# Performance work log

Measured on AMD Instinct MI355X. Metric: run time of the kernel, lower is better.

The kernel has to match this reference:

```python
import jax, jax.numpy as jnp
import numpy as np

N_NODES = 10000
N_EDGES = 160000
DIM = 128
NLAYERS = 3
NBASIS = 16
NSPECIES = 100
CUTOFF = 5.0


def _mlp(x, W1, b1, W2, b2):
    # FullyConnectedNet([hidden, out]) with silu on hidden, linear output
    return jax.nn.silu(x @ W1 + b1) @ W2 + b2


def setup_inputs() -> dict:
    key = jax.random.key(0)
    ks = iter(jax.random.split(key, 64))
    scale = 0.08

    def w(shape):
        return jax.random.normal(next(ks), shape, dtype=jnp.float32) * scale

    inp = {
        "species": jax.random.randint(next(ks), (N_NODES,), 0, NSPECIES, dtype=jnp.int32),
        "edge_src": jnp.sort(jax.random.randint(next(ks), (N_EDGES,), 0, N_NODES, dtype=jnp.int32)),
        "edge_dst": jax.random.randint(next(ks), (N_EDGES,), 0, N_NODES, dtype=jnp.int32),
        "distances": 0.5 + 4.4 * jax.random.uniform(next(ks), (N_EDGES,), dtype=jnp.float32),
        "vec": jax.random.normal(next(ks), (N_EDGES, 3), dtype=jnp.float32),
        "switch": jax.random.uniform(next(ks), (N_EDGES,), dtype=jnp.float32),
        "species_W": w((NSPECIES, DIM)),
        "species_b": w((DIM,)),
        "radial_W": w((NLAYERS, NBASIS, DIM)),
        "radial_b": w((NLAYERS, DIM)),
    }
    for nm, out in [("a", DIM), ("F", 1), ("f", DIM), ("R", DIM), ("r", DIM), ("u", DIM)]:
        inp[nm + "_W1"] = w((NLAYERS, DIM, DIM))
        inp[nm + "_b1"] = w((NLAYERS, DIM))
        inp[nm + "_W2"] = w((NLAYERS, DIM, out))
        inp[nm + "_b2"] = w((NLAYERS, out))
    return inp


def reference(species, edge_src, edge_dst, distances, vec, switch,
              species_W, species_b, radial_W, radial_b,
              a_W1, a_b1, a_W2, a_b2,
              F_W1, F_b1, F_W2, F_b2,
              f_W1, f_b1, f_W2, f_b2,
              R_W1, R_b1, R_W2, R_b2,
              r_W1, r_b1, r_W2, r_b2,
              u_W1, u_b1, u_W2, u_b2):
    N = species.shape[0]
    # species encoding -> species_linear Dense
    xi = jax.nn.one_hot(species, NSPECIES, dtype=jnp.float32) @ species_W + species_b  # (N, dim)
    sw = switch[:, None]                                   # (E, 1)
    dirij = vec / distances[:, None] * sw                  # (E, 3)
    # gaussian radial basis on [0, cutoff]
    centers = jnp.linspace(0.0, CUTOFF, NBASIS, dtype=jnp.float32)
    eta = jnp.float32((NBASIS / CUTOFF) ** 2)
    rb = jnp.exp(-eta * (distances[:, None] - centers) ** 2)  # (E, nbasis)

    fi = None
    di = None
    for l in range(NLAYERS):
        ai = _mlp(xi, a_W1[l], a_b1[l], a_W2[l], a_b2[l])          # (N, dim)
        Dij = rb @ radial_W[l] + radial_b[l]                        # (E, dim)
        mij = ai[edge_src] * ai[edge_dst] * Dij * sw                # (E, dim)
        xi = xi + jax.ops.segment_sum(mij, edge_src, N)
        Fij = _mlp(mij, F_W1[l], F_b1[l], F_W2[l], F_b2[l]) * dirij  # (E, 3)
        fij = _mlp(mij, f_W1[l], f_b1[l], f_W2[l], f_b2[l])[:, :, None] * Fij[:, None, :]  # (E, C, 3)
        fij_sum = jax.ops.segment_sum(fij, edge_src, N)             # (N, C, 3)
        fi = fij_sum if l == 0 else fi + fij_sum
        deltai = _mlp(xi, R_W1[l], R_b1[l], R_W2[l], R_b2[l])[:, :, None] * fi  # (N, C, 3)
        if l == 0:
            di = deltai
        else:
            phi_rij = _mlp(mij, r_W1[l], r_b1[l], r_W2[l], r_b2[l])  # (E, C)
            phi_r = jax.ops.segment_sum(phi_rij * sw, edge_src, N)   # (N, C)
            di = phi_r[:, :, None] * di + deltai
        scal = jnp.sum(fi * di, axis=-1)                             # (N, C)
        dui = -_mlp(xi, u_W1[l], u_b1[l], u_W2[l], u_b2[l]) * scal   # (N, dim) since C == dim
        xi = xi + dui
    return xi
```

## Files before the change

kernel.cpp:

```cpp
#include <hip/hip_runtime.h>
#include <hip/hip_bf16.h>

#define N_NODES 10000
#define N_EDGES 160000
#define DIM     128
#define NBASIS  16
#define LDT     136
#define NFE     (N_NODES*DIM)

typedef __bf16 bf16x8 __attribute__((ext_vector_type(8)));
typedef __bf16 bf16x4 __attribute__((ext_vector_type(4)));
typedef __bf16 bf16x2 __attribute__((ext_vector_type(2)));
typedef float  f32x4  __attribute__((ext_vector_type(4)));

__device__ __forceinline__ float silu_f(float x){
  return x * (1.0f / (1.0f + __expf(-x)));
}
__device__ __forceinline__ f32x4 mfma16(bf16x8 a, bf16x8 b, f32x4 c){
  return __builtin_amdgcn_mfma_f32_16x16x32_bf16(a,b,c,0,0,0);
}


struct WPtrs { const float* p[11]; };

template<bool WITH_R>
__global__ __launch_bounds__(256,2) void mlp_layer(
    int nodeB,
    const __bf16* __restrict__ mij,
    const int*    __restrict__ esrc, const float* __restrict__ dirv,
    const __bf16* __restrict__ fW1z, const float* __restrict__ fb1,
    const __bf16* __restrict__ fW2z, const float* __restrict__ fb2,
    const __bf16* __restrict__ FW1z, const float* __restrict__ Fb1,
    const float*  __restrict__ FW2v, const float* __restrict__ Fb2,
    const __bf16* __restrict__ rW1z, const float* __restrict__ rb1,
    const __bf16* __restrict__ rW2z, const float* __restrict__ rb2,
    const float*  __restrict__ swv,
    float* __restrict__ fiG, float* __restrict__ phiG,
    const float* __restrict__ X,
    const __bf16* __restrict__ RW1z, const float* __restrict__ Rb1,
    const __bf16* __restrict__ RW2z, const float* __restrict__ Rb2,
    const __bf16* __restrict__ uW1z, const float* __restrict__ ub1,
    const __bf16* __restrict__ uW2z, const float* __restrict__ ub2,
    float* __restrict__ Rv, float* __restrict__ uv)
{
  __shared__ __bf16 sH[128*LDT];
  __shared__ __bf16 sW[2][8192];
  __shared__ int    sE[128];
  __shared__ float  sDir[128*3];
  const int tid=threadIdx.x, lane=tid&63, wv=tid>>6, l15=lane&15, quad=lane>>4;

  if ((int)blockIdx.x < nodeB){
    const long row0n = (long)blockIdx.x*64 + wv*16;
    const long rA = row0n + l15;
    const bool okA = rA < N_NODES;

    bf16x8 fa[4];
    #pragma unroll
    for (int kc=0;kc<4;kc++){
      int kb=kc*32+quad*8;
      bf16x8 a;
      #pragma unroll
      for (int i=0;i<8;i++) a[i]=(__bf16)0.f;
      if (okA){
        float4 u0 = *(const float4*)(X + rA*DIM + kb);
        float4 u1 = *(const float4*)(X + rA*DIM + kb + 4);
        a[0]=(__bf16)u0.x;a[1]=(__bf16)u0.y;a[2]=(__bf16)u0.z;a[3]=(__bf16)u0.w;
        a[4]=(__bf16)u1.x;a[5]=(__bf16)u1.y;a[6]=(__bf16)u1.z;a[7]=(__bf16)u1.w;
      }
      fa[kc]=a;
    }

    f32x4 acc[8];
    auto zacc = [&](){
      #pragma unroll
      for (int ni=0;ni<8;++ni) acc[ni]=(f32x4){0.f,0.f,0.f,0.f};
    };
    auto gemmA = [&](const __bf16* __restrict__ Wz){
      #pragma unroll
      for (int kc=0;kc<4;kc++){
        #pragma unroll
        for (int ni=0;ni<8;ni++){
          bf16x8 w = *(const bf16x8*)(Wz + (long)(kc*512 + ni*64 + lane)*8);
          acc[ni]=mfma16(w,fa[kc],acc[ni]);
        }
      }
    };
    auto gemmH = [&](const __bf16* __restrict__ Wz){
      #pragma unroll
      for (int kc=0;kc<4;kc++){
        bf16x8 h0=*(bf16x8*)&sH[(wv*16+l15)*LDT + kc*32 + quad*8];
        #pragma unroll
        for (int ni=0;ni<8;ni++){
          bf16x8 w = *(const bf16x8*)(Wz + (long)(kc*512 + ni*64 + lane)*8);
          acc[ni]=mfma16(w,h0,acc[ni]);
        }
      }
    };
    auto hEpi = [&](const float* __restrict__ b1){
      #pragma unroll
      for (int ni=0;ni<8;++ni){
        int n0 = ni*16 + quad*4;
        float4 bb = *(const float4*)(b1 + n0);
        bf16x4 h;
        h[0]=(__bf16)silu_f(acc[ni][0]+bb.x);
        h[1]=(__bf16)silu_f(acc[ni][1]+bb.y);
        h[2]=(__bf16)silu_f(acc[ni][2]+bb.z);
        h[3]=(__bf16)silu_f(acc[ni][3]+bb.w);
        *(bf16x4*)&sH[(wv*16+l15)*LDT + n0] = h;
      }
    };
    auto cStoreF = [&](const float* __restrict__ b2, float* __restrict__ Y){
      if (okA){
        #pragma unroll
        for (int ni=0;ni<8;++ni){
          int n0 = ni*16 + quad*4;
          float4 bb = *(const float4*)(b2 + n0);
          float4 o;
          o.x=acc[ni][0]+bb.x; o.y=acc[ni][1]+bb.y;
          o.z=acc[ni][2]+bb.z; o.w=acc[ni][3]+bb.w;
          *(float4*)(Y + rA*DIM + n0) = o;
        }
      }
    };

    zacc(); gemmA(RW1z); hEpi(Rb1);
    zacc(); gemmH(RW2z); cStoreF(Rb2, Rv);
    zacc(); gemmA(uW1z); hEpi(ub1);
    zacc(); gemmH(uW2z); cStoreF(ub2, uv);
    return;
  }

  const long row0 = (long)(blockIdx.x - nodeB)*128;
  const int  rloc0 = wv*32 + l15;
  const long rB0 = row0 + rloc0, rB1 = rB0+16;

  if (tid < 32)  *(int4*)&sE[tid*4]    = *(const int4*)(esrc + row0 + tid*4);
  if (tid >= 64 && tid < 160)
    *(float4*)&sDir[(tid-64)*4] = *(const float4*)(dirv + row0*3 + (tid-64)*4);

  bf16x8 fb[2][4];
  #pragma unroll
  for (int kc=0;kc<4;kc++){
    fb[0][kc] = *(const bf16x8*)(mij + rB0*DIM + kc*32 + quad*8);
    fb[1][kc] = *(const bf16x8*)(mij + rB1*DIM + kc*32 + quad*8);
  }
  float swr[2];
  if constexpr (WITH_R){ swr[0]=swv[rB0]; swr[1]=swv[rB1]; }

  f32x4 acc[2][8];
  bf16x8 pre[4];
  float eF[2];

  auto preload = [&](const __bf16* __restrict__ Wz, int half){
    #pragma unroll
    for (int it=0; it<4; ++it)
      pre[it] = *(const bf16x8*)(Wz + (long)(half*1024 + it*256 + tid)*8);
  };
  auto writePre = [&](int b){
    #pragma unroll
    for (int it=0; it<4; ++it)
      *(bf16x8*)&sW[b][(it*256+tid)*8] = pre[it];
  };
  auto zacc = [&](){
    #pragma unroll
    for (int mi=0;mi<2;++mi)
      #pragma unroll
      for (int ni=0;ni<8;++ni) acc[mi][ni]=(f32x4){0.f,0.f,0.f,0.f};
  };
  auto mfmaB = [&](int b, int half){
    #pragma unroll
    for (int k2=0;k2<2;k2++){
      int kc = half*2 + k2;
      #pragma unroll
      for (int ni=0;ni<8;ni++){
        bf16x8 w = *(bf16x8*)&sW[b][(k2*512 + ni*64 + lane)*8];
        acc[0][ni]=mfma16(w,fb[0][kc],acc[0][ni]);
        acc[1][ni]=mfma16(w,fb[1][kc],acc[1][ni]);
      }
    }
  };
  auto mfmaH = [&](int b, int half){
    #pragma unroll
    for (int k2=0;k2<2;k2++){
      int kc = half*2 + k2;
      bf16x8 h0=*(bf16x8*)&sH[(rloc0   )*LDT + kc*32 + quad*8];
      bf16x8 h1=*(bf16x8*)&sH[(rloc0+16)*LDT + kc*32 + quad*8];
      #pragma unroll
      for (int ni=0;ni<8;ni++){
        bf16x8 w = *(bf16x8*)&sW[b][(k2*512 + ni*64 + lane)*8];
        acc[0][ni]=mfma16(w,h0,acc[0][ni]);
        acc[1][ni]=mfma16(w,h1,acc[1][ni]);
      }
    }
  };
  auto fEpi = [&](){
    float fb2v = Fb2[0];
    #pragma unroll
    for (int mi=0;mi<2;++mi){
      float p = 0.f;
      #pragma unroll
      for (int ni=0;ni<8;++ni){
        int n0 = ni*16 + quad*4;
        float4 bb = *(const float4*)(Fb1 + n0);
        float4 w2 = *(const float4*)(FW2v + n0);
        p += silu_f(acc[mi][ni][0]+bb.x)*w2.x;
        p += silu_f(acc[mi][ni][1]+bb.y)*w2.y;
        p += silu_f(acc[mi][ni][2]+bb.z)*w2.z;
        p += silu_f(acc[mi][ni][3]+bb.w)*w2.w;
      }
      p += __shfl_xor(p,16);
      p += __shfl_xor(p,32);
      eF[mi] = p + fb2v;
    }
  };
  auto hEpi = [&](const float* __restrict__ b1){
    #pragma unroll
    for (int mi=0;mi<2;++mi){
      int rl = wv*32 + mi*16 + l15;
      #pragma unroll
      for (int ni=0;ni<8;++ni){
        int n0 = ni*16 + quad*4;
        float4 bb = *(const float4*)(b1 + n0);
        bf16x4 h;
        h[0]=(__bf16)silu_f(acc[mi][ni][0]+bb.x);
        h[1]=(__bf16)silu_f(acc[mi][ni][1]+bb.y);
        h[2]=(__bf16)silu_f(acc[mi][ni][2]+bb.z);
        h[3]=(__bf16)silu_f(acc[mi][ni][3]+bb.w);
        *(bf16x4*)&sH[rl*LDT + n0] = h;
      }
    }
  };
  auto outLDS = [&](const float* __restrict__ b2, const float* mul){
    #pragma unroll
    for (int mi=0;mi<2;++mi){
      int rl = wv*32 + mi*16 + l15;
      #pragma unroll
      for (int ni=0;ni<8;++ni){
        int n0 = ni*16 + quad*4;
        float4 bb = *(const float4*)(b2 + n0);
        bf16x4 o;
        o[0]=(__bf16)((acc[mi][ni][0]+bb.x)*mul[mi]);
        o[1]=(__bf16)((acc[mi][ni][1]+bb.y)*mul[mi]);
        o[2]=(__bf16)((acc[mi][ni][2]+bb.z)*mul[mi]);
        o[3]=(__bf16)((acc[mi][ni][3]+bb.w)*mul[mi]);
        *(bf16x4*)&sH[rl*LDT + n0] = o;
      }
    }
  };
  auto reduceFi = [&](){
    const int d = lane*2;
    float a0=0.f,a1=0.f,a2=0.f,a3=0.f,a4=0.f,a5=0.f;
    int cur = sE[wv*32];
    for (int i=0;i<32;i++){
      int e = wv*32+i;
      int n = sE[e];
      if (n != cur){
        long b = (long)cur*DIM + d;
        atomicAdd(&fiG[0L*NFE + b  ], a0);
        atomicAdd(&fiG[0L*NFE + b+1], a3);
        atomicAdd(&fiG[1L*NFE + b  ], a1);
        atomicAdd(&fiG[1L*NFE + b+1], a4);
        atomicAdd(&fiG[2L*NFE + b  ], a2);
        atomicAdd(&fiG[2L*NFE + b+1], a5);
        a0=a1=a2=a3=a4=a5=0.f; cur=n;
      }
      bf16x2 v = *(bf16x2*)&sH[e*LDT + d];
      float vx=(float)v[0], vy=(float)v[1];
      float d0=sDir[e*3+0], d1=sDir[e*3+1], d2=sDir[e*3+2];
      a0+=vx*d0; a1+=vx*d1; a2+=vx*d2;
      a3+=vy*d0; a4+=vy*d1; a5+=vy*d2;
    }
    long b = (long)cur*DIM + d;
    atomicAdd(&fiG[0L*NFE + b  ], a0);
    atomicAdd(&fiG[0L*NFE + b+1], a3);
    atomicAdd(&fiG[1L*NFE + b  ], a1);
    atomicAdd(&fiG[1L*NFE + b+1], a4);
    atomicAdd(&fiG[2L*NFE + b  ], a2);
    atomicAdd(&fiG[2L*NFE + b+1], a5);
  };
  auto reducePhi = [&](){
    const int d = lane*2;
    float a0=0.f,a1=0.f;
    int cur = sE[wv*32];
    for (int i=0;i<32;i++){
      int e = wv*32+i;
      int n = sE[e];
      if (n != cur){
        atomicAdd(&phiG[(long)cur*DIM + d  ], a0);
        atomicAdd(&phiG[(long)cur*DIM + d+1], a1);
        a0=a1=0.f; cur=n;
      }
      bf16x2 v = *(bf16x2*)&sH[e*LDT + d];
      a0 += (float)v[0]; a1 += (float)v[1];
    }
    atomicAdd(&phiG[(long)cur*DIM + d  ], a0);
    atomicAdd(&phiG[(long)cur*DIM + d+1], a1);
  };

  preload(FW1z,0); writePre(0);
  __syncthreads();
  preload(FW1z,1);
  zacc(); mfmaB(0,0);
  writePre(1);
  __syncthreads();
  preload(fW1z,0);
  mfmaB(1,1);
  writePre(0);
  __syncthreads();
  preload(fW1z,1);
  fEpi();
  zacc(); mfmaB(0,0);
  writePre(1);
  __syncthreads();
  preload(fW2z,0);
  mfmaB(1,1);
  writePre(0);
  __syncthreads();
  preload(fW2z,1);
  hEpi(fb1);
  zacc(); mfmaH(0,0);
  writePre(1);
  __syncthreads();
  if constexpr (WITH_R) preload(rW1z,0);
  mfmaH(1,1);
  outLDS(fb2, eF);
  reduceFi();

  if constexpr (WITH_R){
    writePre(0);
    __syncthreads();
    preload(rW1z,1);
    zacc(); mfmaB(0,0);
    writePre(1);
    __syncthreads();
    preload(rW2z,0);
    mfmaB(1,1);
    writePre(0);
    __syncthreads();
    preload(rW2z,1);
    hEpi(rb1);
    zacc(); mfmaH(0,0);
    writePre(1);
    __syncthreads();
    mfmaH(1,1);
    outLDS(rb2, swr);
    reducePhi();
  }
}

__global__ __launch_bounds__(64,4) void mlp_a(
    const float* __restrict__ X,
    const __bf16* __restrict__ W1z, const float* __restrict__ b1,
    const __bf16* __restrict__ W2z, const float* __restrict__ b2,
    __bf16* __restrict__ Y)
{
  __shared__ __bf16 sH[16*LDT];
  const int lane=threadIdx.x, l15=lane&15, quad=lane>>4;
  const long row0=(long)blockIdx.x*16;
  const long rA=row0+l15;

  bf16x8 fa[4];
  #pragma unroll
  for (int kc=0;kc<4;kc++){
    int kb=kc*32+quad*8;
    float4 u0 = *(const float4*)(X + rA*DIM + kb);
    float4 u1 = *(const float4*)(X + rA*DIM + kb + 4);
    bf16x8 a;
    a[0]=(__bf16)u0.x;a[1]=(__bf16)u0.y;a[2]=(__bf16)u0.z;a[3]=(__bf16)u0.w;
    a[4]=(__bf16)u1.x;a[5]=(__bf16)u1.y;a[6]=(__bf16)u1.z;a[7]=(__bf16)u1.w;
    fa[kc]=a;
  }

  f32x4 acc[8];
  #pragma unroll
  for (int ni=0;ni<8;++ni) acc[ni]=(f32x4){0.f,0.f,0.f,0.f};
  #pragma unroll
  for (int kc=0;kc<4;kc++){
    #pragma unroll
    for (int ni=0;ni<8;ni++){
      bf16x8 w = *(const bf16x8*)(W1z + (long)(kc*512 + ni*64 + lane)*8);
      acc[ni]=mfma16(w,fa[kc],acc[ni]);
    }
  }
  #pragma unroll
  for (int ni=0;ni<8;++ni){
    int n0 = ni*16 + quad*4;
    float4 bb = *(const float4*)(b1 + n0);
    bf16x4 h;
    h[0]=(__bf16)silu_f(acc[ni][0]+bb.x);
    h[1]=(__bf16)silu_f(acc[ni][1]+bb.y);
    h[2]=(__bf16)silu_f(acc[ni][2]+bb.z);
    h[3]=(__bf16)silu_f(acc[ni][3]+bb.w);
    *(bf16x4*)&sH[l15*LDT + n0] = h;
  }
  #pragma unroll
  for (int ni=0;ni<8;++ni) acc[ni]=(f32x4){0.f,0.f,0.f,0.f};
  #pragma unroll
  for (int kc=0;kc<4;kc++){
    bf16x8 h0=*(bf16x8*)&sH[l15*LDT + kc*32 + quad*8];
    #pragma unroll
    for (int ni=0;ni<8;ni++){
      bf16x8 w = *(const bf16x8*)(W2z + (long)(kc*512 + ni*64 + lane)*8);
      acc[ni]=mfma16(w,h0,acc[ni]);
    }
  }
  #pragma unroll
  for (int ni=0;ni<8;++ni){
    int n0 = ni*16 + quad*4;
    float4 bb = *(const float4*)(b2 + n0);
    bf16x4 o;
    o[0]=(__bf16)(acc[ni][0]+bb.x);
    o[1]=(__bf16)(acc[ni][1]+bb.y);
    o[2]=(__bf16)(acc[ni][2]+bb.z);
    o[3]=(__bf16)(acc[ni][3]+bb.w);
    *(bf16x4*)(Y + rA*DIM + n0) = o;
  }
}

__global__ __launch_bounds__(256) void setup_all(
    WPtrs wp, __bf16* __restrict__ wt,
    const int* __restrict__ species, const float* __restrict__ spW,
    const float* __restrict__ spB, float* __restrict__ xi, float* __restrict__ fi,
    float* __restrict__ phi,
    const float* __restrict__ dist, const float* __restrict__ vec,
    const float* __restrict__ swv, float* __restrict__ dir, float* __restrict__ rb)
{
  const int b = blockIdx.x, tid = threadIdx.x;
  if (b < 33){
    int t = b/3, l = b%3;
    const float* src = wp.p[t] + (size_t)l*16384;
    __bf16* out = wt + (size_t)b*16384;
    for (int it=0; it<8; ++it){
      int fi_ = it*256 + tid;
      int kc = fi_>>9, ni = (fi_>>6)&7, lane = fi_&63;
      int n  = ni*16 + (lane&15);
      int k0 = kc*32 + (lane>>4)*8;
      bf16x8 v;
      #pragma unroll
      for (int j=0;j<8;++j) v[j] = (__bf16)src[(k0+j)*DIM + n];
      *(bf16x8*)(out + (size_t)fi_*8) = v;
    }
  } else if (b < 33 + 5000){
    int idx = (b-33)*256 + tid;
    int n = idx >> 7, d = idx & 127;
    xi[idx] = spW[species[n]*DIM + d] + spB[d];
    phi[idx] = 0.f;
    fi[idx] = 0.f;
    fi[NFE + idx] = 0.f;
    fi[2L*NFE + idx] = 0.f;
  } else {
    int e = (b-5033)*256 + tid;
    if (e < N_EDGES){
      float d = dist[e];
      float s = swv[e];
      float inv = s / d;
      dir[e*3+0] = vec[e*3+0]*inv;
      dir[e*3+1] = vec[e*3+1]*inv;
      dir[e*3+2] = vec[e*3+2]*inv;
      const float eta = (16.0f/5.0f)*(16.0f/5.0f);
      #pragma unroll
      for (int j=0;j<NBASIS;j++){
        float c = (float)j * (5.0f/15.0f);
        float t2 = d - c;
        rb[e*NBASIS + j] = __expf(-eta*t2*t2);
      }
    }
  }
}

__global__ __launch_bounds__(256) void mij_segsum(
    const __bf16* __restrict__ ai, const int* __restrict__ esrc, const int* __restrict__ edst,
    const float* __restrict__ swv, const float* __restrict__ rb,
    const float* __restrict__ radW, const float* __restrict__ radB,
    __bf16* __restrict__ mij, float* __restrict__ xi)
{
  __shared__ float sRb[64*NBASIS];
  __shared__ int   sS[64], sD[64];
  __shared__ float sSw[64];
  int tid = threadIdx.x;
  int e0 = blockIdx.x * 64;
  *(float4*)(sRb + tid*4) = *(const float4*)(rb + (long)e0*NBASIS + tid*4);
  if (tid < 64){
    sS[tid]  = esrc[e0+tid];
    sD[tid]  = edst[e0+tid];
    sSw[tid] = swv[e0+tid];
  }
  const int wv = tid>>6, lane = tid&63;
  const int d = lane*2;
  float2 rw[NBASIS];
  #pragma unroll
  for (int j=0;j<NBASIS;j++)
    rw[j] = *(const float2*)(radW + j*DIM + d);
  float2 rB = *(const float2*)(radB + d);
  __syncthreads();

  float sx=0.f, sy=0.f;
  int cur = sS[wv*16];
  #pragma unroll
  for (int i=0;i<16;i++){
    int el = wv*16 + i;
    int n = sS[el];
    if (n != cur){
      atomicAdd(&xi[(long)cur*DIM+d  ], sx);
      atomicAdd(&xi[(long)cur*DIM+d+1], sy);
      sx=0.f; sy=0.f; cur=n;
    }
    bf16x2 as = *(const bf16x2*)(ai + (long)n*DIM + d);
    bf16x2 ad = *(const bf16x2*)(ai + (long)sD[el]*DIM + d);
    float acc0 = 0.f, acc1 = 0.f;
    #pragma unroll
    for (int j=0;j<NBASIS;j++){
      float rbv = sRb[el*NBASIS+j];
      acc0 += rbv*rw[j].x;
      acc1 += rbv*rw[j].y;
    }
    float sw_ = sSw[el];
    float m0 = (float)as[0]*(float)ad[0]*(acc0+rB.x)*sw_;
    float m1 = (float)as[1]*(float)ad[1]*(acc1+rB.y)*sw_;
    bf16x2 m; m[0]=(__bf16)m0; m[1]=(__bf16)m1;
    *(bf16x2*)(mij + (long)(e0+el)*DIM + d) = m;
    sx += m0; sy += m1;
  }
  atomicAdd(&xi[(long)cur*DIM+d  ], sx);
  atomicAdd(&xi[(long)cur*DIM+d+1], sy);
}

__global__ __launch_bounds__(256) void node_update(
    const float* __restrict__ Rv, const float* __restrict__ uv,
    float* __restrict__ fi, float* __restrict__ di, float* __restrict__ xi,
    float* __restrict__ phi, float* __restrict__ out, int layer)
{
  long idx = (long)blockIdx.x*256 + threadIdx.x;
  float f0 = fi[idx];
  float f1 = fi[NFE + idx];
  float f2 = fi[2L*NFE + idx];
  float phi_v = (layer > 0) ? phi[idx] : 0.f;
  float Rv_ = Rv[idx];
  float fv[3] = {f0,f1,f2};
  float sc = 0.f;
  #pragma unroll
  for (int k=0;k<3;k++){
    float delta = Rv_*fv[k];
    float dv = (layer==0) ? delta : phi_v*di[(long)k*NFE + idx] + delta;
    di[(long)k*NFE + idx] = dv;
    sc += fv[k]*dv;
  }
  float nx = xi[idx] - uv[idx]*sc;
  xi[idx] = nx;
  phi[idx] = 0.f;
  if (layer == 2) out[idx] = nx;
}

extern "C" void kernel_launch(void* const* d_in, const int* in_sizes, int n_in,
                              void* d_out, int out_size, void* d_ws, size_t ws_size,
                              hipStream_t stream) {
  const int*   species = (const int*)  d_in[0];
  const int*   esrc    = (const int*)  d_in[1];
  const int*   edst    = (const int*)  d_in[2];
  const float* dist    = (const float*)d_in[3];
  const float* vec     = (const float*)d_in[4];
  const float* swv     = (const float*)d_in[5];
  const float* spW     = (const float*)d_in[6];
  const float* spB     = (const float*)d_in[7];
  const float* radW    = (const float*)d_in[8];
  const float* radB    = (const float*)d_in[9];
  const float* aW1=(const float*)d_in[10], *aB1=(const float*)d_in[11], *aW2=(const float*)d_in[12], *aB2=(const float*)d_in[13];
  const float* FW1=(const float*)d_in[14], *FB1=(const float*)d_in[15], *FW2=(const float*)d_in[16], *FB2=(const float*)d_in[17];
  const float* fW1=(const float*)d_in[18], *fB1=(const float*)d_in[19], *fW2=(const float*)d_in[20], *fB2=(const float*)d_in[21];
  const float* RW1=(const float*)d_in[22], *RB1=(const float*)d_in[23], *RW2=(const float*)d_in[24], *RB2=(const float*)d_in[25];
  const float* rW1=(const float*)d_in[26], *rB1=(const float*)d_in[27], *rW2=(const float*)d_in[28], *rB2=(const float*)d_in[29];
  const float* uW1=(const float*)d_in[30], *uB1=(const float*)d_in[31], *uW2=(const float*)d_in[32], *uB2=(const float*)d_in[33];

  const long NF = (long)N_NODES*DIM;
  const long EF = (long)N_EDGES*DIM;
  float* ws   = (float*)d_ws;
  float* xi   = ws;
  float* Rv   = xi   + NF;
  float* uv   = Rv   + NF;
  float* phi  = uv   + NF;
  float* fi   = phi  + NF;
  float* di   = fi   + 3*NF;
  float* dir  = di   + 3*NF;
  float* rb   = dir  + 3L*N_EDGES;
  char* bp = (char*)(rb + 16L*N_EDGES);
  size_t off = ((size_t)(bp - (char*)d_ws) + 15) & ~(size_t)15;
  __bf16* ai   = (__bf16*)((char*)d_ws + off);
  __bf16* mij  = ai  + NF;
  __bf16* wt   = mij + EF;

  WPtrs wp;
  wp.p[0]=aW1; wp.p[1]=aW2; wp.p[2]=FW1; wp.p[3]=fW1; wp.p[4]=fW2;
  wp.p[5]=RW1; wp.p[6]=RW2; wp.p[7]=rW1; wp.p[8]=rW2; wp.p[9]=uW1; wp.p[10]=uW2;

  setup_all<<<5658, 256, 0, stream>>>(wp, wt,
                                      species, spW, spB, xi, fi, phi,
                                      dist, vec, swv, dir, rb);

  const int nodeB = (N_NODES + 63)/64;
  const int edgeB = N_EDGES/128;
  #define WT(t,l) (wt + (size_t)((t)*3+(l))*16384)

  for (int l=0;l<3;l++){
    const long bo = (long)l*DIM;

    mlp_a<<<N_NODES/16, 64, 0, stream>>>(xi, WT(0,l), aB1+bo, WT(1,l), aB2+bo, ai);
    mij_segsum<<<N_EDGES/64, 256, 0, stream>>>(ai, esrc, edst, swv, rb,
                                               radW + (long)l*NBASIS*DIM, radB + bo,
                                               mij, xi);
    if (l == 0)
      mlp_layer<false><<<nodeB+edgeB, 256, 0, stream>>>(
          nodeB, mij, esrc, dir,
          WT(3,l), fB1+bo, WT(4,l), fB2+bo,
          WT(2,l), FB1+bo, FW2+(long)l*DIM, FB2+l,
          nullptr, nullptr, nullptr, nullptr, nullptr,
          fi, phi,
          xi, WT(5,l), RB1+bo, WT(6,l), RB2+bo,
          WT(9,l), uB1+bo, WT(10,l), uB2+bo, Rv, uv);
    else
      mlp_layer<true><<<nodeB+edgeB, 256, 0, stream>>>(
          nodeB, mij, esrc, dir,
          WT(3,l), fB1+bo, WT(4,l), fB2+bo,
          WT(2,l), FB1+bo, FW2+(long)l*DIM, FB2+l,
          WT(7,l), rB1+bo, WT(8,l), rB2+bo, swv,
          fi, phi,
          xi, WT(5,l), RB1+bo, WT(6,l), RB2+bo,
          WT(9,l), uB1+bo, WT(10,l), uB2+bo, Rv, uv);
    node_update<<<5000, 256, 0, stream>>>(Rv, uv, fi, di, xi, phi,
                                          (float*)d_out, l);
  }
}
```

Baseline: 502.3 us.

## Read MLP weights directly from global memory and drop LDS double-buffering

The edge-MLP path no longer stages weight tiles through a double-buffered shared-memory array with per-stage barriers. Each wave now loads weight fragments straight from global memory, relying on L1/L2 caching. This cuts shared-memory use so the launch bound can rise to 4 blocks per CU and removes most barriers. The cost is that every wave fetches the full weight matrices separately, which adds cache traffic. Direction vectors are also padded to float4 in shared memory so each edge needs one vector load, and one barrier is added after the index and direction staging.

```diff
diff --git a/kernel.cpp b/kernel.cpp
--- a/kernel.cpp
+++ b/kernel.cpp
@@ -24,7 +24,7 @@
 struct WPtrs { const float* p[11]; };
 
 template<bool WITH_R>
-__global__ __launch_bounds__(256,2) void mlp_layer(
+__global__ __launch_bounds__(256,4) void mlp_layer(
     int nodeB,
     const __bf16* __restrict__ mij,
     const int*    __restrict__ esrc, const float* __restrict__ dirv,
@@ -44,9 +44,8 @@
     float* __restrict__ Rv, float* __restrict__ uv)
 {
   __shared__ __bf16 sH[128*LDT];
-  __shared__ __bf16 sW[2][8192];
   __shared__ int    sE[128];
-  __shared__ float  sDir[128*3];
+  __shared__ float  sDir[128*4];
   const int tid=threadIdx.x, lane=tid&63, wv=tid>>6, l15=lane&15, quad=lane>>4;
 
   if ((int)blockIdx.x < nodeB){
@@ -134,9 +133,13 @@
   const int  rloc0 = wv*32 + l15;
   const long rB0 = row0 + rloc0, rB1 = rB0+16;
 
-  if (tid < 32)  *(int4*)&sE[tid*4]    = *(const int4*)(esrc + row0 + tid*4);
-  if (tid >= 64 && tid < 160)
-    *(float4*)&sDir[(tid-64)*4] = *(const float4*)(dirv + row0*3 + (tid-64)*4);
+  if (tid < 32)  *(int4*)&sE[tid*4] = *(const int4*)(esrc + row0 + tid*4);
+  if (tid >= 128){
+    int t = tid - 128;
+    long e3 = (row0 + t)*3;
+    float d0 = dirv[e3+0], d1 = dirv[e3+1], d2 = dirv[e3+2];
+    *(float4*)&sDir[t*4] = (float4){d0,d1,d2,0.f};
+  }
 
   bf16x8 fb[2][4];
   #pragma unroll
@@ -147,47 +150,36 @@
   float swr[2];
   if constexpr (WITH_R){ swr[0]=swv[rB0]; swr[1]=swv[rB1]; }
 
+  __syncthreads();
+
   f32x4 acc[2][8];
-  bf16x8 pre[4];
   float eF[2];
 
-  auto preload = [&](const __bf16* __restrict__ Wz, int half){
-    #pragma unroll
-    for (int it=0; it<4; ++it)
-      pre[it] = *(const bf16x8*)(Wz + (long)(half*1024 + it*256 + tid)*8);
-  };
-  auto writePre = [&](int b){
-    #pragma unroll
-    for (int it=0; it<4; ++it)
-      *(bf16x8*)&sW[b][(it*256+tid)*8] = pre[it];
-  };
   auto zacc = [&](){
     #pragma unroll
     for (int mi=0;mi<2;++mi)
       #pragma unroll
       for (int ni=0;ni<8;++ni) acc[mi][ni]=(f32x4){0.f,0.f,0.f,0.f};
   };
-  auto mfmaB = [&](int b, int half){
-    #pragma unroll
-    for (int k2=0;k2<2;k2++){
-      int kc = half*2 + k2;
+  auto gemmG = [&](const __bf16* __restrict__ Wz){
+    #pragma unroll
+    for (int kc=0;kc<4;kc++){
       #pragma unroll
       for (int ni=0;ni<8;ni++){
-        bf16x8 w = *(bf16x8*)&sW[b][(k2*512 + ni*64 + lane)*8];
+        bf16x8 w = *(const bf16x8*)(Wz + (long)(kc*512 + ni*64 + lane)*8);
         acc[0][ni]=mfma16(w,fb[0][kc],acc[0][ni]);
         acc[1][ni]=mfma16(w,fb[1][kc],acc[1][ni]);
       }
     }
   };
-  auto mfmaH = [&](int b, int half){
-    #pragma unroll
-    for (int k2=0;k2<2;k2++){
-      int kc = half*2 + k2;
+  auto gemmHG = [&](const __bf16* __restrict__ Wz){
+    #pragma unroll
+    for (int kc=0;kc<4;kc++){
       bf16x8 h0=*(bf16x8*)&sH[(rloc0   )*LDT + kc*32 + quad*8];
       bf16x8 h1=*(bf16x8*)&sH[(rloc0+16)*LDT + kc*32 + quad*8];
       #pragma unroll
       for (int ni=0;ni<8;ni++){
-        bf16x8 w = *(bf16x8*)&sW[b][(k2*512 + ni*64 + lane)*8];
+        bf16x8 w = *(const bf16x8*)(Wz + (long)(kc*512 + ni*64 + lane)*8);
         acc[0][ni]=mfma16(w,h0,acc[0][ni]);
         acc[1][ni]=mfma16(w,h1,acc[1][ni]);
       }
@@ -266,9 +258,9 @@
       }
       bf16x2 v = *(bf16x2*)&sH[e*LDT + d];
       float vx=(float)v[0], vy=(float)v[1];
-      float d0=sDir[e*3+0], d1=sDir[e*3+1], d2=sDir[e*3+2];
-      a0+=vx*d0; a1+=vx*d1; a2+=vx*d2;
-      a3+=vy*d0; a4+=vy*d1; a5+=vy*d2;
+      float4 dv = *(float4*)&sDir[e*4];
+      a0+=vx*dv.x; a1+=vx*dv.y; a2+=vx*dv.z;
+      a3+=vy*dv.x; a4+=vy*dv.y; a5+=vy*dv.z;
     }
     long b = (long)cur*DIM + d;
     atomicAdd(&fiG[0L*NFE + b  ], a0);
@@ -297,54 +289,12 @@
     atomicAdd(&phiG[(long)cur*DIM + d+1], a1);
   };
 
-  preload(FW1z,0); writePre(0);
-  __syncthreads();
-  preload(FW1z,1);
-  zacc(); mfmaB(0,0);
-  writePre(1);
-  __syncthreads();
-  preload(fW1z,0);
-  mfmaB(1,1);
-  writePre(0);
-  __syncthreads();
-  preload(fW1z,1);
-  fEpi();
-  zacc(); mfmaB(0,0);
-  writePre(1);
-  __syncthreads();
-  preload(fW2z,0);
-  mfmaB(1,1);
-  writePre(0);
-  __syncthreads();
-  preload(fW2z,1);
-  hEpi(fb1);
-  zacc(); mfmaH(0,0);
-  writePre(1);
-  __syncthreads();
-  if constexpr (WITH_R) preload(rW1z,0);
-  mfmaH(1,1);
-  outLDS(fb2, eF);
-  reduceFi();
-
+  zacc(); gemmG(FW1z); fEpi();
+  zacc(); gemmG(fW1z); hEpi(fb1);
+  zacc(); gemmHG(fW2z); outLDS(fb2, eF); reduceFi();
   if constexpr (WITH_R){
-    writePre(0);
-    __syncthreads();
-    preload(rW1z,1);
-    zacc(); mfmaB(0,0);
-    writePre(1);
-    __syncthreads();
-    preload(rW2z,0);
-    mfmaB(1,1);
-    writePre(0);
-    __syncthreads();
-    preload(rW2z,1);
-    hEpi(rb1);
-    zacc(); mfmaH(0,0);
-    writePre(1);
-    __syncthreads();
-    mfmaH(1,1);
-    outLDS(rb2, swr);
-    reducePhi();
+    zacc(); gemmG(rW1z); hEpi(rb1);
+    zacc(); gemmHG(rW2z); outLDS(rb2, swr); reducePhi();
   }
 }
 
```

Measured after the change: 694.1 us. +38.2%, slower.

## Fuse message computation into edge MLP and node MLPs into the node update

Applied to the files above, without the earlier changes.

The per-edge message (radial projection, ai gather, switch) is now computed inside the edge MLP kernel and kept in shared memory, with its segment-sum into xi done there too. This removes the separate mij kernel and the bf16 mij round-trip through global memory. The node-side R and u MLPs, the elementwise node update, and the next layer's a-MLP are merged into a single node kernel, which drops the Rv/uv buffers and two launches per layer. In exchange, node work no longer runs concurrently with edge blocks in the same launch, and the edge kernel uses more shared memory and registers, which may lower occupancy.

```diff
diff --git a/kernel.cpp b/kernel.cpp
--- a/kernel.cpp
+++ b/kernel.cpp
@@ -24,128 +24,90 @@
 struct WPtrs { const float* p[11]; };
 
 template<bool WITH_R>
-__global__ __launch_bounds__(256,2) void mlp_layer(
-    int nodeB,
-    const __bf16* __restrict__ mij,
-    const int*    __restrict__ esrc, const float* __restrict__ dirv,
+__global__ __launch_bounds__(256,2) void mlp_edge(
+    const __bf16* __restrict__ ai,
+    const int*    __restrict__ esrc, const int* __restrict__ edst,
+    const float*  __restrict__ swv,  const float* __restrict__ rbG,
+    const float*  __restrict__ radW, const float* __restrict__ radB,
+    const float*  __restrict__ dirv,
     const __bf16* __restrict__ fW1z, const float* __restrict__ fb1,
     const __bf16* __restrict__ fW2z, const float* __restrict__ fb2,
     const __bf16* __restrict__ FW1z, const float* __restrict__ Fb1,
     const float*  __restrict__ FW2v, const float* __restrict__ Fb2,
     const __bf16* __restrict__ rW1z, const float* __restrict__ rb1,
     const __bf16* __restrict__ rW2z, const float* __restrict__ rb2,
-    const float*  __restrict__ swv,
-    float* __restrict__ fiG, float* __restrict__ phiG,
-    const float* __restrict__ X,
-    const __bf16* __restrict__ RW1z, const float* __restrict__ Rb1,
-    const __bf16* __restrict__ RW2z, const float* __restrict__ Rb2,
-    const __bf16* __restrict__ uW1z, const float* __restrict__ ub1,
-    const __bf16* __restrict__ uW2z, const float* __restrict__ ub2,
-    float* __restrict__ Rv, float* __restrict__ uv)
+    float* __restrict__ xiG, float* __restrict__ fiG, float* __restrict__ phiG)
 {
   __shared__ __bf16 sH[128*LDT];
   __shared__ __bf16 sW[2][8192];
+  __shared__ float  sRb[128*NBASIS];
+  __shared__ float  sDir[128*4];
   __shared__ int    sE[128];
-  __shared__ float  sDir[128*3];
+  __shared__ int    sD[128];
+  __shared__ float  sSw[128];
   const int tid=threadIdx.x, lane=tid&63, wv=tid>>6, l15=lane&15, quad=lane>>4;
-
-  if ((int)blockIdx.x < nodeB){
-    const long row0n = (long)blockIdx.x*64 + wv*16;
-    const long rA = row0n + l15;
-    const bool okA = rA < N_NODES;
-
-    bf16x8 fa[4];
-    #pragma unroll
-    for (int kc=0;kc<4;kc++){
-      int kb=kc*32+quad*8;
-      bf16x8 a;
-      #pragma unroll
-      for (int i=0;i<8;i++) a[i]=(__bf16)0.f;
-      if (okA){
-        float4 u0 = *(const float4*)(X + rA*DIM + kb);
-        float4 u1 = *(const float4*)(X + rA*DIM + kb + 4);
-        a[0]=(__bf16)u0.x;a[1]=(__bf16)u0.y;a[2]=(__bf16)u0.z;a[3]=(__bf16)u0.w;
-        a[4]=(__bf16)u1.x;a[5]=(__bf16)u1.y;a[6]=(__bf16)u1.z;a[7]=(__bf16)u1.w;
-      }
-      fa[kc]=a;
-    }
-
-    f32x4 acc[8];
-    auto zacc = [&](){
-      #pragma unroll
-      for (int ni=0;ni<8;++ni) acc[ni]=(f32x4){0.f,0.f,0.f,0.f};
-    };
-    auto gemmA = [&](const __bf16* __restrict__ Wz){
-      #pragma unroll
-      for (int kc=0;kc<4;kc++){
-        #pragma unroll
-        for (int ni=0;ni<8;ni++){
-          bf16x8 w = *(const bf16x8*)(Wz + (long)(kc*512 + ni*64 + lane)*8);
-          acc[ni]=mfma16(w,fa[kc],acc[ni]);
-        }
-      }
-    };
-    auto gemmH = [&](const __bf16* __restrict__ Wz){
-      #pragma unroll
-      for (int kc=0;kc<4;kc++){
-        bf16x8 h0=*(bf16x8*)&sH[(wv*16+l15)*LDT + kc*32 + quad*8];
-        #pragma unroll
-        for (int ni=0;ni<8;ni++){
-          bf16x8 w = *(const bf16x8*)(Wz + (long)(kc*512 + ni*64 + lane)*8);
-          acc[ni]=mfma16(w,h0,acc[ni]);
-        }
-      }
-    };
-    auto hEpi = [&](const float* __restrict__ b1){
-      #pragma unroll
-      for (int ni=0;ni<8;++ni){
-        int n0 = ni*16 + quad*4;
-        float4 bb = *(const float4*)(b1 + n0);
-        bf16x4 h;
-        h[0]=(__bf16)silu_f(acc[ni][0]+bb.x);
-        h[1]=(__bf16)silu_f(acc[ni][1]+bb.y);
-        h[2]=(__bf16)silu_f(acc[ni][2]+bb.z);
-        h[3]=(__bf16)silu_f(acc[ni][3]+bb.w);
-        *(bf16x4*)&sH[(wv*16+l15)*LDT + n0] = h;
-      }
-    };
-    auto cStoreF = [&](const float* __restrict__ b2, float* __restrict__ Y){
-      if (okA){
-        #pragma unroll
-        for (int ni=0;ni<8;++ni){
-          int n0 = ni*16 + quad*4;
-          float4 bb = *(const float4*)(b2 + n0);
-          float4 o;
-          o.x=acc[ni][0]+bb.x; o.y=acc[ni][1]+bb.y;
-          o.z=acc[ni][2]+bb.z; o.w=acc[ni][3]+bb.w;
-          *(float4*)(Y + rA*DIM + n0) = o;
-        }
-      }
-    };
-
-    zacc(); gemmA(RW1z); hEpi(Rb1);
-    zacc(); gemmH(RW2z); cStoreF(Rb2, Rv);
-    zacc(); gemmA(uW1z); hEpi(ub1);
-    zacc(); gemmH(uW2z); cStoreF(ub2, uv);
-    return;
-  }
-
-  const long row0 = (long)(blockIdx.x - nodeB)*128;
+  const long row0 = (long)blockIdx.x*128;
   const int  rloc0 = wv*32 + l15;
-  const long rB0 = row0 + rloc0, rB1 = rB0+16;
-
-  if (tid < 32)  *(int4*)&sE[tid*4]    = *(const int4*)(esrc + row0 + tid*4);
-  if (tid >= 64 && tid < 160)
-    *(float4*)&sDir[(tid-64)*4] = *(const float4*)(dirv + row0*3 + (tid-64)*4);
+
+  if (tid >= 128){
+    int t = tid - 128;
+    long e3 = (row0 + t)*3;
+    float d0 = dirv[e3+0], d1 = dirv[e3+1], d2 = dirv[e3+2];
+    *(float4*)&sDir[t*4] = (float4){d0,d1,d2,0.f};
+  }
+  if (lane < 32){
+    int el = wv*32 + lane; long e = row0 + el;
+    sE[el] = esrc[e]; sD[el] = edst[e]; sSw[el] = swv[e];
+  }
+  {
+    const float* src = rbG + (row0 + wv*32)*NBASIS;
+    *(float4*)&sRb[wv*512 + lane*8    ] = *(const float4*)(src + lane*8);
+    *(float4*)&sRb[wv*512 + lane*8 + 4] = *(const float4*)(src + lane*8 + 4);
+  }
+
+  const int d = lane*2;
+  {
+    float2 rw[NBASIS];
+    #pragma unroll
+    for (int j=0;j<NBASIS;j++) rw[j] = *(const float2*)(radW + j*DIM + d);
+    float2 rBv = *(const float2*)(radB + d);
+    float sx=0.f, sy=0.f;
+    int cur = sE[wv*32];
+    for (int i=0;i<32;i++){
+      int el = wv*32 + i;
+      int n = sE[el];
+      if (n != cur){
+        atomicAdd(&xiG[(long)cur*DIM+d  ], sx);
+        atomicAdd(&xiG[(long)cur*DIM+d+1], sy);
+        sx=0.f; sy=0.f; cur=n;
+      }
+      bf16x2 as_ = *(const bf16x2*)(ai + (long)n*DIM + d);
+      bf16x2 ad_ = *(const bf16x2*)(ai + (long)sD[el]*DIM + d);
+      float a0=0.f, a1=0.f;
+      #pragma unroll
+      for (int j=0;j<NBASIS;j++){
+        float rv = sRb[el*NBASIS+j];
+        a0 += rv*rw[j].x; a1 += rv*rw[j].y;
+      }
+      float sw_ = sSw[el];
+      float m0 = (float)as_[0]*(float)ad_[0]*(a0+rBv.x)*sw_;
+      float m1 = (float)as_[1]*(float)ad_[1]*(a1+rBv.y)*sw_;
+      bf16x2 m; m[0]=(__bf16)m0; m[1]=(__bf16)m1;
+      *(bf16x2*)&sH[el*LDT + d] = m;
+      sx += m0; sy += m1;
+    }
+    atomicAdd(&xiG[(long)cur*DIM+d  ], sx);
+    atomicAdd(&xiG[(long)cur*DIM+d+1], sy);
+  }
 
   bf16x8 fb[2][4];
   #pragma unroll
   for (int kc=0;kc<4;kc++){
-    fb[0][kc] = *(const bf16x8*)(mij + rB0*DIM + kc*32 + quad*8);
-    fb[1][kc] = *(const bf16x8*)(mij + rB1*DIM + kc*32 + quad*8);
+    fb[0][kc] = *(bf16x8*)&sH[(rloc0   )*LDT + kc*32 + quad*8];
+    fb[1][kc] = *(bf16x8*)&sH[(rloc0+16)*LDT + kc*32 + quad*8];
   }
   float swr[2];
-  if constexpr (WITH_R){ swr[0]=swv[rB0]; swr[1]=swv[rB1]; }
+  if constexpr (WITH_R){ swr[0]=sSw[rloc0]; swr[1]=sSw[rloc0+16]; }
 
   f32x4 acc[2][8];
   bf16x8 pre[4];
@@ -248,7 +210,6 @@
     }
   };
   auto reduceFi = [&](){
-    const int d = lane*2;
     float a0=0.f,a1=0.f,a2=0.f,a3=0.f,a4=0.f,a5=0.f;
     int cur = sE[wv*32];
     for (int i=0;i<32;i++){
@@ -266,9 +227,9 @@
       }
       bf16x2 v = *(bf16x2*)&sH[e*LDT + d];
       float vx=(float)v[0], vy=(float)v[1];
-      float d0=sDir[e*3+0], d1=sDir[e*3+1], d2=sDir[e*3+2];
-      a0+=vx*d0; a1+=vx*d1; a2+=vx*d2;
-      a3+=vy*d0; a4+=vy*d1; a5+=vy*d2;
+      float4 dv = *(float4*)&sDir[e*4];
+      a0+=vx*dv.x; a1+=vx*dv.y; a2+=vx*dv.z;
+      a3+=vy*dv.x; a4+=vy*dv.y; a5+=vy*dv.z;
     }
     long b = (long)cur*DIM + d;
     atomicAdd(&fiG[0L*NFE + b  ], a0);
@@ -279,7 +240,6 @@
     atomicAdd(&fiG[2L*NFE + b+1], a5);
   };
   auto reducePhi = [&](){
-    const int d = lane*2;
     float a0=0.f,a1=0.f;
     int cur = sE[wv*32];
     for (int i=0;i<32;i++){
@@ -348,6 +308,157 @@
   }
 }
 
+__global__ __launch_bounds__(256,2) void node_fused(
+    const float* __restrict__ X,
+    const __bf16* __restrict__ RW1z, const float* __restrict__ Rb1,
+    const __bf16* __restrict__ RW2z, const float* __restrict__ Rb2,
+    const __bf16* __restrict__ uW1z, const float* __restrict__ ub1,
+    const __bf16* __restrict__ uW2z, const float* __restrict__ ub2,
+    const __bf16* __restrict__ aW1z, const float* __restrict__ ab1,
+    const __bf16* __restrict__ aW2z, const float* __restrict__ ab2,
+    float* __restrict__ fi, float* __restrict__ di,
+    float* __restrict__ phi, float* __restrict__ xi,
+    __bf16* __restrict__ ai, float* __restrict__ out, int layer)
+{
+  __shared__ __bf16 sH[64*LDT];
+  const int tid=threadIdx.x, lane=tid&63, wv=tid>>6, l15=lane&15, quad=lane>>4;
+  const long rA = (long)blockIdx.x*64 + wv*16 + l15;
+  const bool okA = rA < N_NODES;
+  const int rl = wv*16 + l15;
+
+  bf16x8 fa[4];
+  #pragma unroll
+  for (int kc=0;kc<4;kc++){
+    int kb=kc*32+quad*8;
+    bf16x8 a;
+    #pragma unroll
+    for (int i=0;i<8;i++) a[i]=(__bf16)0.f;
+    if (okA){
+      float4 u0 = *(const float4*)(X + rA*DIM + kb);
+      float4 u1 = *(const float4*)(X + rA*DIM + kb + 4);
+      a[0]=(__bf16)u0.x;a[1]=(__bf16)u0.y;a[2]=(__bf16)u0.z;a[3]=(__bf16)u0.w;
+      a[4]=(__bf16)u1.x;a[5]=(__bf16)u1.y;a[6]=(__bf16)u1.z;a[7]=(__bf16)u1.w;
+    }
+    fa[kc]=a;
+  }
+
+  f32x4 acc[8];
+  auto zacc = [&](){
+    #pragma unroll
+    for (int ni=0;ni<8;++ni) acc[ni]=(f32x4){0.f,0.f,0.f,0.f};
+  };
+  auto gemmA = [&](const __bf16* __restrict__ Wz, const bf16x8* f){
+    #pragma unroll
+    for (int kc=0;kc<4;kc++){
+      #pragma unroll
+      for (int ni=0;ni<8;ni++){
+        bf16x8 w = *(const bf16x8*)(Wz + (long)(kc*512 + ni*64 + lane)*8);
+        acc[ni]=mfma16(w,f[kc],acc[ni]);
+      }
+    }
+  };
+  auto gemmH = [&](const __bf16* __restrict__ Wz){
+    #pragma unroll
+    for (int kc=0;kc<4;kc++){
+      bf16x8 h0=*(bf16x8*)&sH[rl*LDT + kc*32 + quad*8];
+      #pragma unroll
+      for (int ni=0;ni<8;ni++){
+        bf16x8 w = *(const bf16x8*)(Wz + (long)(kc*512 + ni*64 + lane)*8);
+        acc[ni]=mfma16(w,h0,acc[ni]);
+      }
+    }
+  };
+  auto hEpi = [&](const float* __restrict__ b1){
+    #pragma unroll
+    for (int ni=0;ni<8;++ni){
+      int n0 = ni*16 + quad*4;
+      float4 bb = *(const float4*)(b1 + n0);
+      bf16x4 h;
+      h[0]=(__bf16)silu_f(acc[ni][0]+bb.x);
+      h[1]=(__bf16)silu_f(acc[ni][1]+bb.y);
+      h[2]=(__bf16)silu_f(acc[ni][2]+bb.z);
+      h[3]=(__bf16)silu_f(acc[ni][3]+bb.w);
+      *(bf16x4*)&sH[rl*LDT + n0] = h;
+    }
+  };
+
+  f32x4 Rv4[8], Uv4[8];
+  zacc(); gemmA(RW1z, fa); hEpi(Rb1);
+  zacc(); gemmH(RW2z);
+  #pragma unroll
+  for (int ni=0;ni<8;++ni) Rv4[ni]=acc[ni];
+  zacc(); gemmA(uW1z, fa); hEpi(ub1);
+  zacc(); gemmH(uW2z);
+  #pragma unroll
+  for (int ni=0;ni<8;++ni) Uv4[ni]=acc[ni];
+
+  if (okA){
+    #pragma unroll
+    for (int ni=0;ni<8;++ni){
+      int n0 = ni*16 + quad*4;
+      long idx = rA*DIM + n0;
+      float4 rb2v = *(const float4*)(Rb2 + n0);
+      float4 ub2v = *(const float4*)(ub2 + n0);
+      float4 f0 = *(const float4*)(fi + idx);
+      float4 f1 = *(const float4*)(fi + NFE + idx);
+      float4 f2 = *(const float4*)(fi + 2L*NFE + idx);
+      float4 xv = *(const float4*)(X + idx);
+      float4 ph = (layer>0) ? *(const float4*)(phi + idx) : (float4){0,0,0,0};
+      float4 e0 = (layer>0) ? *(const float4*)(di + idx)          : (float4){0,0,0,0};
+      float4 e1 = (layer>0) ? *(const float4*)(di + NFE + idx)    : (float4){0,0,0,0};
+      float4 e2 = (layer>0) ? *(const float4*)(di + 2L*NFE + idx) : (float4){0,0,0,0};
+      float4 nd0, nd1, nd2, nx;
+      #pragma unroll
+      for (int j=0;j<4;++j){
+        float Rvv = Rv4[ni][j] + ((const float*)&rb2v)[j];
+        float uvv = Uv4[ni][j] + ((const float*)&ub2v)[j];
+        float d0v = ((const float*)&ph)[j]*((const float*)&e0)[j] + Rvv*((const float*)&f0)[j];
+        float d1v = ((const float*)&ph)[j]*((const float*)&e1)[j] + Rvv*((const float*)&f1)[j];
+        float d2v = ((const float*)&ph)[j]*((const float*)&e2)[j] + Rvv*((const float*)&f2)[j];
+        float sc = ((const float*)&f0)[j]*d0v + ((const float*)&f1)[j]*d1v
+                 + ((const float*)&f2)[j]*d2v;
+        ((float*)&nd0)[j]=d0v; ((float*)&nd1)[j]=d1v; ((float*)&nd2)[j]=d2v;
+        ((float*)&nx)[j] = ((const float*)&xv)[j] - uvv*sc;
+      }
+      *(float4*)(di + idx)          = nd0;
+      *(float4*)(di + NFE + idx)    = nd1;
+      *(float4*)(di + 2L*NFE + idx) = nd2;
+      if (layer == 2){
+        *(float4*)(out + idx) = nx;
+      } else {
+        *(float4*)(xi + idx) = nx;
+        *(float4*)(phi + idx) = (float4){0,0,0,0};
+        bf16x4 h;
+        h[0]=(__bf16)nx.x; h[1]=(__bf16)nx.y;
+        h[2]=(__bf16)nx.z; h[3]=(__bf16)nx.w;
+        *(bf16x4*)&sH[rl*LDT + n0] = h;
+      }
+    }
+  }
+
+  if (layer < 2){
+    bf16x8 fa2[4];
+    #pragma unroll
+    for (int kc=0;kc<4;kc++)
+      fa2[kc] = *(bf16x8*)&sH[rl*LDT + kc*32 + quad*8];
+    zacc(); gemmA(aW1z, fa2); hEpi(ab1);
+    zacc(); gemmH(aW2z);
+    if (okA){
+      #pragma unroll
+      for (int ni=0;ni<8;++ni){
+        int n0 = ni*16 + quad*4;
+        float4 bb = *(const float4*)(ab2 + n0);
+        bf16x4 o;
+        o[0]=(__bf16)(acc[ni][0]+bb.x);
+        o[1]=(__bf16)(acc[ni][1]+bb.y);
+        o[2]=(__bf16)(acc[ni][2]+bb.z);
+        o[3]=(__bf16)(acc[ni][3]+bb.w);
+        *(bf16x4*)(ai + rA*DIM + n0) = o;
+      }
+    }
+  }
+}
+
 __global__ __launch_bounds__(64,4) void mlp_a(
     const float* __restrict__ X,
     const __bf16* __restrict__ W1z, const float* __restrict__ b1,
@@ -468,89 +579,6 @@
   }
 }
 
-__global__ __launch_bounds__(256) void mij_segsum(
-    const __bf16* __restrict__ ai, const int* __restrict__ esrc, const int* __restrict__ edst,
-    const float* __restrict__ swv, const float* __restrict__ rb,
-    const float* __restrict__ radW, const float* __restrict__ radB,
-    __bf16* __restrict__ mij, float* __restrict__ xi)
-{
-  __shared__ float sRb[64*NBASIS];
-  __shared__ int   sS[64], sD[64];
-  __shared__ float sSw[64];
-  int tid = threadIdx.x;
-  int e0 = blockIdx.x * 64;
-  *(float4*)(sRb + tid*4) = *(const float4*)(rb + (long)e0*NBASIS + tid*4);
-  if (tid < 64){
-    sS[tid]  = esrc[e0+tid];
-    sD[tid]  = edst[e0+tid];
-    sSw[tid] = swv[e0+tid];
-  }
-  const int wv = tid>>6, lane = tid&63;
-  const int d = lane*2;
-  float2 rw[NBASIS];
-  #pragma unroll
-  for (int j=0;j<NBASIS;j++)
-    rw[j] = *(const float2*)(radW + j*DIM + d);
-  float2 rB = *(const float2*)(radB + d);
-  __syncthreads();
-
-  float sx=0.f, sy=0.f;
-  int cur = sS[wv*16];
-  #pragma unroll
-  for (int i=0;i<16;i++){
-    int el = wv*16 + i;
-    int n = sS[el];
-    if (n != cur){
-      atomicAdd(&xi[(long)cur*DIM+d  ], sx);
-      atomicAdd(&xi[(long)cur*DIM+d+1], sy);
-      sx=0.f; sy=0.f; cur=n;
-    }
-    bf16x2 as = *(const bf16x2*)(ai + (long)n*DIM + d);
-    bf16x2 ad = *(const bf16x2*)(ai + (long)sD[el]*DIM + d);
-    float acc0 = 0.f, acc1 = 0.f;
-    #pragma unroll
-    for (int j=0;j<NBASIS;j++){
-      float rbv = sRb[el*NBASIS+j];
-      acc0 += rbv*rw[j].x;
-      acc1 += rbv*rw[j].y;
-    }
-    float sw_ = sSw[el];
-    float m0 = (float)as[0]*(float)ad[0]*(acc0+rB.x)*sw_;
-    float m1 = (float)as[1]*(float)ad[1]*(acc1+rB.y)*sw_;
-    bf16x2 m; m[0]=(__bf16)m0; m[1]=(__bf16)m1;
-    *(bf16x2*)(mij + (long)(e0+el)*DIM + d) = m;
-    sx += m0; sy += m1;
-  }
-  atomicAdd(&xi[(long)cur*DIM+d  ], sx);
-  atomicAdd(&xi[(long)cur*DIM+d+1], sy);
-}
-
-__global__ __launch_bounds__(256) void node_update(
-    const float* __restrict__ Rv, const float* __restrict__ uv,
-    float* __restrict__ fi, float* __restrict__ di, float* __restrict__ xi,
-    float* __restrict__ phi, float* __restrict__ out, int layer)
-{
-  long idx = (long)blockIdx.x*256 + threadIdx.x;
-  float f0 = fi[idx];
-  float f1 = fi[NFE + idx];
-  float f2 = fi[2L*NFE + idx];
-  float phi_v = (layer > 0) ? phi[idx] : 0.f;
-  float Rv_ = Rv[idx];
-  float fv[3] = {f0,f1,f2};
-  float sc = 0.f;
-  #pragma unroll
-  for (int k=0;k<3;k++){
-    float delta = Rv_*fv[k];
-    float dv = (layer==0) ? delta : phi_v*di[(long)k*NFE + idx] + delta;
-    di[(long)k*NFE + idx] = dv;
-    sc += fv[k]*dv;
-  }
-  float nx = xi[idx] - uv[idx]*sc;
-  xi[idx] = nx;
-  phi[idx] = 0.f;
-  if (layer == 2) out[idx] = nx;
-}
-
 extern "C" void kernel_launch(void* const* d_in, const int* in_sizes, int n_in,
                               void* d_out, int out_size, void* d_ws, size_t ws_size,
                               hipStream_t stream) {
@@ -572,12 +600,9 @@
   const float* uW1=(const float*)d_in[30], *uB1=(const float*)d_in[31], *uW2=(const float*)d_in[32], *uB2=(const float*)d_in[33];
 
   const long NF = (long)N_NODES*DIM;
-  const long EF = (long)N_EDGES*DIM;
   float* ws   = (float*)d_ws;
   float* xi   = ws;
-  float* Rv   = xi   + NF;
-  float* uv   = Rv   + NF;
-  float* phi  = uv   + NF;
+  float* phi  = xi   + NF;
   float* fi   = phi  + NF;
   float* di   = fi   + 3*NF;
   float* dir  = di   + 3*NF;
@@ -585,8 +610,7 @@
   char* bp = (char*)(rb + 16L*N_EDGES);
   size_t off = ((size_t)(bp - (char*)d_ws) + 15) & ~(size_t)15;
   __bf16* ai   = (__bf16*)((char*)d_ws + off);
-  __bf16* mij  = ai  + NF;
-  __bf16* wt   = mij + EF;
+  __bf16* wt   = ai + NF;
 
   WPtrs wp;
   wp.p[0]=aW1; wp.p[1]=aW2; wp.p[2]=FW1; wp.p[3]=fW1; wp.p[4]=fW2;
@@ -596,36 +620,39 @@
                                       species, spW, spB, xi, fi, phi,
                                       dist, vec, swv, dir, rb);
 
+  #define WT(t,l) (wt + (size_t)((t)*3+(l))*16384)
+
+  mlp_a<<<N_NODES/16, 64, 0, stream>>>(xi, WT(0,0), aB1, WT(1,0), aB2, ai);
+
+  const int edgeB = N_EDGES/128;
   const int nodeB = (N_NODES + 63)/64;
-  const int edgeB = N_EDGES/128;
-  #define WT(t,l) (wt + (size_t)((t)*3+(l))*16384)
 
   for (int l=0;l<3;l++){
     const long bo = (long)l*DIM;
 
-    mlp_a<<<N_NODES/16, 64, 0, stream>>>(xi, WT(0,l), aB1+bo, WT(1,l), aB2+bo, ai);
-    mij_segsum<<<N_EDGES/64, 256, 0, stream>>>(ai, esrc, edst, swv, rb,
-                                               radW + (long)l*NBASIS*DIM, radB + bo,
-                                               mij, xi);
     if (l == 0)
-      mlp_layer<false><<<nodeB+edgeB, 256, 0, stream>>>(
-          nodeB, mij, esrc, dir,
+      mlp_edge<false><<<edgeB, 256, 0, stream>>>(
+          ai, esrc, edst, swv, rb,
+          radW + (long)l*NBASIS*DIM, radB + bo, dir,
           WT(3,l), fB1+bo, WT(4,l), fB2+bo,
           WT(2,l), FB1+bo, FW2+(long)l*DIM, FB2+l,
-          nullptr, nullptr, nullptr, nullptr, nullptr,
-          fi, phi,
-          xi, WT(5,l), RB1+bo, WT(6,l), RB2+bo,
-          WT(9,l), uB1+bo, WT(10,l), uB2+bo, Rv, uv);
+          nullptr, nullptr, nullptr, nullptr,
+          xi, fi, phi);
     else
-      mlp_layer<true><<<nodeB+edgeB, 256, 0, stream>>>(
-          nodeB, mij, esrc, dir,
+      mlp_edge<true><<<edgeB, 256, 0, stream>>>(
+          ai, esrc, edst, swv, rb,
+          radW + (long)l*NBASIS*DIM, radB + bo, dir,
           WT(3,l), fB1+bo, WT(4,l), fB2+bo,
           WT(2,l), FB1+bo, FW2+(long)l*DIM, FB2+l,
-          WT(7,l), rB1+bo, WT(8,l), rB2+bo, swv,
-          fi, phi,
-          xi, WT(5,l), RB1+bo, WT(6,l), RB2+bo,
-          WT(9,l), uB1+bo, WT(10,l), uB2+bo, Rv, uv);
-    node_update<<<5000, 256, 0, stream>>>(Rv, uv, fi, di, xi, phi,
-                                          (float*)d_out, l);
+          WT(7,l), rB1+bo, WT(8,l), rB2+bo,
+          xi, fi, phi);
+
+    int ln = (l < 2) ? (l+1) : 0;
+    node_fused<<<nodeB, 256, 0, stream>>>(
+        xi,
+        WT(5,l), RB1+bo, WT(6,l), RB2+bo,
+        WT(9,l), uB1+bo, WT(10,l), uB2+bo,
+        WT(0,ln), aB1+(long)ln*DIM, WT(1,ln), aB2+(long)ln*DIM,
+        fi, di, phi, xi, ai, (float*)d_out, l);
   }
 }
```

After: 612.8 us. 22.0% more time.
